# Kernel optimization log

Measured on AMD Instinct MI355X. Metric: run time of the kernel, lower is better.

Reference implementation:

```python
import jax, jax.numpy as jnp
import numpy as np

B, H, V, E, TOPK = 65536, 768, 512, 8, 2
D = H + V  # combined_dim = 1280


def setup_inputs() -> dict:
    key = jax.random.key(0)
    ks = jax.random.split(key, 12)
    def rn(k, sh, scale):
        return jax.random.normal(k, sh, dtype=jnp.float32) * scale
    return {
        "text_features": rn(ks[0], (B, H), 1.0),
        "video_features": rn(ks[1], (B, V), 1.0),
        # 8 stacked experts: 1280->256->128->1
        "exp_w1": rn(ks[2], (E, D, 256), 0.02), "exp_b1": jnp.zeros((E, 256), jnp.float32),
        "exp_w2": rn(ks[3], (E, 256, 128), 0.05), "exp_b2": jnp.zeros((E, 128), jnp.float32),
        "exp_w3": rn(ks[4], (E, 128, 1), 0.08), "exp_b3": jnp.zeros((E, 1), jnp.float32),
        # text router: 768->256->8
        "txt_r_w1": rn(ks[5], (H, 256), 0.03), "txt_r_b1": jnp.zeros((256,), jnp.float32),
        "txt_r_w2": rn(ks[6], (256, E), 0.06), "txt_r_b2": jnp.zeros((E,), jnp.float32),
        # video router: 512->256->8
        "vid_r_w1": rn(ks[7], (V, 256), 0.04), "vid_r_b1": jnp.zeros((256,), jnp.float32),
        "vid_r_w2": rn(ks[8], (256, E), 0.06), "vid_r_b2": jnp.zeros((E,), jnp.float32),
    }


def _router(x, w1, b1, w2, b2):
    return jax.nn.relu(x @ w1 + b1) @ w2 + b2  # [B, E]


def _aggregate(expert_outs, idx, weights):
    # expert_outs: [B, E]; idx/weights: [B, TOPK]
    chosen = jnp.take_along_axis(expert_outs, idx, axis=1)  # [B, TOPK]
    return jnp.sum(weights * chosen, axis=-1, keepdims=True)  # [B, 1]


def reference(text_features, video_features,
              exp_w1, exp_b1, exp_w2, exp_b2, exp_w3, exp_b3,
              txt_r_w1, txt_r_b1, txt_r_w2, txt_r_b2,
              vid_r_w1, vid_r_b1, vid_r_w2, vid_r_b2):
    combined = jnp.concatenate([text_features, video_features], axis=-1)  # [B, D]

    t_logits = _router(text_features, txt_r_w1, txt_r_b1, txt_r_w2, txt_r_b2)
    v_logits = _router(video_features, vid_r_w1, vid_r_b1, vid_r_w2, vid_r_b2)

    t_val, t_idx = jax.lax.top_k(t_logits, TOPK)
    v_val, v_idx = jax.lax.top_k(v_logits, TOPK)
    t_w = jax.nn.softmax(t_val, axis=-1)
    v_w = jax.nn.softmax(v_val, axis=-1)

    # Dense evaluation of all 8 experts (matches original Python loop, vectorized)
    h1 = jax.nn.relu(jnp.einsum('bd,edh->beh', combined, exp_w1) + exp_b1)  # [B,E,256]
    h2 = jax.nn.relu(jnp.einsum('beh,ehf->bef', h1, exp_w2) + exp_b2)       # [B,E,128]
    eo = jax.nn.sigmoid(jnp.einsum('bef,efo->beo', h2, exp_w3) + exp_b3)    # [B,E,1]
    eo = eo[:, :, 0]  # [B, E]

    text_conf = _aggregate(eo, t_idx, t_w)   # [B, 1]
    video_conf = _aggregate(eo, v_idx, v_w)  # [B, 1]
    return text_conf, video_conf
```

## Files before the change

### kernel.cpp

```cpp
#include <hip/hip_runtime.h>
#include <stdint.h>
#include <math.h>

#define B_N 65536
#define H_N 768
#define V_N 512
#define D_N 1280
#define E_N 8
#define N1  256
#define N2  128

#define W1E (E_N*D_N*N1)
#define W2E (E_N*N1*N2)
#define TRE (24*16*512)
#define VRE (16*16*512)

#define DELTA    5e-3f
#define FLAG_CAP 8192

typedef __attribute__((ext_vector_type(8))) short bf16x8;
typedef __attribute__((ext_vector_type(4))) float f32x4;

__device__ __forceinline__ unsigned short f2bf(float f){
  union{float f;uint32_t u;}v; v.f=f;
  uint32_t r = v.u + 0x7FFFu + ((v.u>>16)&1u);
  return (unsigned short)(r>>16);
}
__device__ __forceinline__ float bf2f(unsigned short s){
  union{uint32_t u; float f;}v; v.u = ((uint32_t)s)<<16; return v.f;
}

__global__ void convert_weights(const float* __restrict__ w1,
                                const float* __restrict__ w2,
                                const float* __restrict__ tw1,
                                const float* __restrict__ vw1,
                                unsigned short* __restrict__ w1b,
                                unsigned short* __restrict__ w2b,
                                unsigned short* __restrict__ t_hi,
                                unsigned short* __restrict__ t_lo,
                                unsigned short* __restrict__ v_hi,
                                unsigned short* __restrict__ v_lo,
                                int* __restrict__ counters){
  int i = blockIdx.x*256 + threadIdx.x;
  if (i < 16) counters[i] = 0;
  if (i < W1E){
    int tile = i >> 9, r = i & 511;
    int l = r >> 3, j = r & 7;
    int gt = tile & 15, t2 = tile >> 4;
    int ks = t2 % 40, e = t2 / 40;
    int k = ks*32 + 8*(l>>4) + j;
    int n = gt*16 + (l&15);
    w1b[i] = f2bf(w1[((size_t)e*D_N + k)*N1 + n]);
    return;
  }
  i -= W1E;
  if (i < W2E){
    int tile = i >> 9, r = i & 511;
    int l = r >> 3, j = r & 7;
    int ft = tile & 7, t2 = tile >> 3;
    int ks = t2 & 7, e = t2 >> 3;
    int k = ks*32 + 8*(l>>4) + j;
    int f = ft*16 + (l&15);
    w2b[i] = f2bf(w2[((size_t)e*N1 + k)*N2 + f]);
    return;
  }
  i -= W2E;
  if (i < TRE){
    int tile = i >> 9, r = i & 511;
    int l = r >> 3, j = r & 7;
    int gt = tile & 15, ks = tile >> 4;
    int k = ks*32 + 8*(l>>4) + j;
    int n = gt*16 + (l&15);
    float x = tw1[(size_t)k*N1 + n];
    unsigned short h = f2bf(x);
    t_hi[i] = h;
    t_lo[i] = f2bf(x - bf2f(h));
    return;
  }
  i -= TRE;
  if (i < VRE){
    int tile = i >> 9, r = i & 511;
    int l = r >> 3, j = r & 7;
    int gt = tile & 15, ks = tile >> 4;
    int k = ks*32 + 8*(l>>4) + j;
    int n = gt*16 + (l&15);
    float x = vw1[(size_t)k*N1 + n];
    unsigned short h = f2bf(x);
    v_hi[i] = h;
    v_lo[i] = f2bf(x - bf2f(h));
  }
}

__global__ __launch_bounds__(512,4) void router_mfma(
    const float* __restrict__ text, const float* __restrict__ video,
    const unsigned short* __restrict__ t_hi, const unsigned short* __restrict__ t_lo,
    const unsigned short* __restrict__ v_hi, const unsigned short* __restrict__ v_lo,
    const float* __restrict__ tb1, const float* __restrict__ tw2, const float* __restrict__ tb2,
    const float* __restrict__ vb1, const float* __restrict__ vw2, const float* __restrict__ vb2,
    int* __restrict__ selIdx, float2* __restrict__ selW,
    int* __restrict__ flags, int* __restrict__ counters)
{
  __shared__ union {
    unsigned short a[4*2560];
    float h[64*264];
  } s;
  __shared__ float W2s[256*8];

  const int tid = threadIdx.x;
  const int rt = blockIdx.x >> 10;
  const int r0 = (blockIdx.x & 1023) * 64;
  const float* X = rt ? video : text;
  const unsigned short* Whi = rt ? v_hi : t_hi;
  const unsigned short* Wlo = rt ? v_lo : t_lo;
  const float* b1 = rt ? vb1 : tb1;
  const float* W2 = rt ? vw2 : tw2;
  const float* b2 = rt ? vb2 : tb2;
  const int K  = rt ? V_N : H_N;
  const int NK = K >> 5;

  const int w = tid >> 6, l = tid & 63;
  const int mw = w & 1, nw = w >> 1;
  const int srow = tid >> 3, skq = (tid & 7) * 4;

  for (int i = tid; i < 2048; i += 512) W2s[i] = W2[i];

  f32x4 acc[2][4];
#pragma unroll
  for (int a=0;a<2;a++)
#pragma unroll
    for (int b=0;b<4;b++) acc[a][b] = (f32x4){0.f,0.f,0.f,0.f};

  const float* xrow = X + (size_t)(r0 + srow)*K + skq;
  float4 areg = *(const float4*)xrow;

  for (int ks = 0; ks < NK; ++ks){
    {
      unsigned short* dhi = s.a + (ks&1)*2560 + srow*40 + skq;
      unsigned short* dlo = s.a + (2+(ks&1))*2560 + srow*40 + skq;
      ushort4 uh, ul;
      uh.x = f2bf(areg.x); ul.x = f2bf(areg.x - bf2f(uh.x));
      uh.y = f2bf(areg.y); ul.y = f2bf(areg.y - bf2f(uh.y));
      uh.z = f2bf(areg.z); ul.z = f2bf(areg.z - bf2f(uh.z));
      uh.w = f2bf(areg.w); ul.w = f2bf(areg.w - bf2f(uh.w));
      *(ushort4*)dhi = uh;
      *(ushort4*)dlo = ul;
    }
    if (ks + 1 < NK) areg = *(const float4*)(xrow + (ks+1)*32);
    __syncthreads();

    bf16x8 bh[4], bl[4];
#pragma unroll
    for (int nt=0;nt<4;nt++){
      size_t off = (size_t)(ks*16 + nw*4 + nt)*512 + l*8;
      bh[nt] = *(const bf16x8*)(Whi + off);
      bl[nt] = *(const bf16x8*)(Wlo + off);
    }
    bf16x8 ah[2], al[2];
    const unsigned short* ahi = s.a + (ks&1)*2560;
    const unsigned short* alo = s.a + (2+(ks&1))*2560;
#pragma unroll
    for (int mt=0;mt<2;mt++){
      int ro = (mw*32 + mt*16 + (l&15))*40 + 8*(l>>4);
      ah[mt] = *(const bf16x8*)(ahi + ro);
      al[mt] = *(const bf16x8*)(alo + ro);
    }
#pragma unroll
    for (int mt=0;mt<2;mt++)
#pragma unroll
      for (int nt=0;nt<4;nt++){
        acc[mt][nt] = __builtin_amdgcn_mfma_f32_16x16x32_bf16(ah[mt], bh[nt], acc[mt][nt], 0,0,0);
        acc[mt][nt] = __builtin_amdgcn_mfma_f32_16x16x32_bf16(ah[mt], bl[nt], acc[mt][nt], 0,0,0);
        acc[mt][nt] = __builtin_amdgcn_mfma_f32_16x16x32_bf16(al[mt], bh[nt], acc[mt][nt], 0,0,0);
      }
  }
  __syncthreads();

#pragma unroll
  for (int mt=0;mt<2;mt++){
#pragma unroll
    for (int nt=0;nt<4;nt++){
      int n = nw*64 + nt*16 + (l&15);
      float b1v = b1[n];
#pragma unroll
      for (int i=0;i<4;i++){
        int row = mw*32 + mt*16 + (l>>4)*4 + i;
        float v = acc[mt][nt][i] + b1v;
        s.h[row*264 + n] = v > 0.f ? v : 0.f;
      }
    }
  }
  __syncthreads();

  {
    const int r = tid >> 3, j = tid & 7;
    float part[8];
#pragma unroll
    for (int e=0;e<8;e++) part[e] = 0.f;
    for (int q=0;q<32;q++){
      int n = j + 8*q;
      float hv = s.h[r*264 + n];
#pragma unroll
      for (int e=0;e<8;e++) part[e] += hv * W2s[n*8 + e];
    }
#pragma unroll
    for (int m=1;m<=4;m<<=1)
#pragma unroll
      for (int e=0;e<8;e++) part[e] += __shfl_xor(part[e], m);

    if (j == 0){
      int row = r0 + r;
      float L[8];
#pragma unroll
      for (int e=0;e<8;e++) L[e] = part[e] + b2[e];
      int i0 = 0; float v0 = L[0];
#pragma unroll
      for (int e=1;e<8;e++) if (L[e] > v0){ v0 = L[e]; i0 = e; }
      int i1 = -1; float v1 = -1e30f;
#pragma unroll
      for (int e=0;e<8;e++) if (e != i0 && L[e] > v1){ v1 = L[e]; i1 = e; }
      float v2 = -1e30f;
#pragma unroll
      for (int e=0;e<8;e++) if (e != i0 && e != i1 && L[e] > v2) v2 = L[e];
      if (v1 - v2 < DELTA){
        int idx = atomicAdd(&counters[0], 1);
        if (idx < FLAG_CAP) flags[idx] = (rt<<16) | row;
      }
      float e1 = expf(v1 - v0);
      float invd = 1.f/(1.f + e1);
      selIdx[rt*B_N + row] = i0 | (i1 << 8);
      selW[rt*B_N + row] = make_float2(invd, e1*invd);
    }
  }
}

__global__ __launch_bounds__(256) void router_exact(
    const float* __restrict__ text, const float* __restrict__ video,
    const float* __restrict__ tw1, const float* __restrict__ tb1,
    const float* __restrict__ tw2, const float* __restrict__ tb2,
    const float* __restrict__ vw1, const float* __restrict__ vb1,
    const float* __restrict__ vw2, const float* __restrict__ vb2,
    int* __restrict__ selIdx, float2* __restrict__ selW,
    const int* __restrict__ flags, const int* __restrict__ counters)
{
  int nf = counters[0]; if (nf > FLAG_CAP) nf = FLAG_CAP;
  if ((int)blockIdx.x >= nf) return;
  int code = flags[blockIdx.x];
  int rt = code >> 16, row = code & 0xFFFF;
  const float* X  = rt ? video : text;
  const float* W1 = rt ? vw1 : tw1;
  const float* b1 = rt ? vb1 : tb1;
  const float* W2 = rt ? vw2 : tw2;
  const float* b2 = rt ? vb2 : tb2;
  const int K = rt ? V_N : H_N;

  __shared__ float xs[H_N];
  __shared__ double red[4][8];
  const int tid = threadIdx.x;
  for (int k = tid; k < K; k += 256) xs[k] = X[(size_t)row*K + k];
  __syncthreads();

  double sAcc = 0.0;
  for (int k = 0; k < K; ++k)
    sAcc += (double)xs[k] * (double)W1[(size_t)k*N1 + tid];
  sAcc += (double)b1[tid];
  double h = sAcc > 0.0 ? sAcc : 0.0;

  double p[8];
#pragma unroll
  for (int e=0;e<8;e++) p[e] = h * (double)W2[tid*8 + e];
#pragma unroll
  for (int m=1;m<=32;m<<=1)
#pragma unroll
    for (int e=0;e<8;e++) p[e] += __shfl_xor(p[e], m);
  if ((tid & 63) == 0){
#pragma unroll
    for (int e=0;e<8;e++) red[tid>>6][e] = p[e];
  }
  __syncthreads();
  if (tid == 0){
    double L[8];
#pragma unroll
    for (int e=0;e<8;e++) L[e] = red[0][e]+red[1][e]+red[2][e]+red[3][e] + (double)b2[e];
    int i0 = 0; double v0 = L[0];
#pragma unroll
    for (int e=1;e<8;e++) if (L[e] > v0){ v0 = L[e]; i0 = e; }
    int i1 = -1; double v1 = -1e300;
#pragma unroll
    for (int e=0;e<8;e++) if (e != i0 && L[e] > v1){ v1 = L[e]; i1 = e; }
    double e1 = exp(v1 - v0);
    double invd = 1.0/(1.0 + e1);
    selIdx[rt*B_N + row] = i0 | (i1 << 8);
    selW[rt*B_N + row] = make_float2((float)invd, (float)(e1*invd));
  }
}

__global__ __launch_bounds__(256) void bucket_build(
    const int* __restrict__ selIdx, int* __restrict__ bucket,
    int* __restrict__ counters)
{
  __shared__ int lcnt[8], lbase[8], lpos[8];
  const int tid = threadIdx.x;
  const int row = blockIdx.x*256 + tid;
  if (tid < 8){ lcnt[tid] = 0; lpos[tid] = 0; }
  __syncthreads();
  int st = selIdx[row], sv = selIdx[B_N + row];
  int mask = (1<<(st&7)) | (1<<((st>>8)&7)) | (1<<(sv&7)) | (1<<((sv>>8)&7));
#pragma unroll
  for (int e=0;e<8;e++) if ((mask>>e)&1) atomicAdd(&lcnt[e], 1);
  __syncthreads();
  if (tid < 8) lbase[tid] = atomicAdd(&counters[8+tid], lcnt[tid]);
  __syncthreads();
#pragma unroll
  for (int e=0;e<8;e++)
    if ((mask>>e)&1){
      int p = atomicAdd(&lpos[e], 1);
      bucket[e*B_N + lbase[e] + p] = row;
    }
}

__global__ __launch_bounds__(512) void expert_sparse(
    const float* __restrict__ text, const float* __restrict__ video,
    const unsigned short* __restrict__ w1b, const float* __restrict__ b1,
    const unsigned short* __restrict__ w2b, const float* __restrict__ b2,
    const float* __restrict__ w3, const float* __restrict__ b3,
    const int* __restrict__ bucket, const int* __restrict__ counters,
    float* __restrict__ eo)
{
  __shared__ __align__(16) unsigned short As[4096];
  __shared__ __align__(16) unsigned short h1s[32768];
  __shared__ int rl[128];

  const int tid = threadIdx.x;
  const int e = blockIdx.x & 7;
  const int t = blockIdx.x >> 3;
  const int n_e = counters[8 + e];
  if (t*128 >= n_e) return;

  if (tid < 128){
    int idx = t*128 + tid;
    rl[tid] = (idx < n_e) ? bucket[e*B_N + idx] : -1;
  }
  __syncthreads();

  const int w = tid >> 6, l = tid & 63;
  const int mw = w & 1, nw = w >> 1;

  const int sridx = rl[(tid>>6)*16 + (l&15)];
  const int srr = sridx < 0 ? 0 : sridx;
  const float* tb = text  + (size_t)srr*H_N + (l>>4)*8;
  const float* vb = video + (size_t)srr*V_N + (l>>4)*8;

  f32x4 acc[4][4];
#pragma unroll
  for (int a=0;a<4;a++)
#pragma unroll
    for (int b=0;b<4;b++) acc[a][b] = (f32x4){0.f,0.f,0.f,0.f};

  const unsigned short* w1e = w1b + (size_t)e*40*16*512;

  float4 fa0 = *(const float4*)tb;
  float4 fa1 = *(const float4*)(tb + 4);
  bf16x8 bfc[4];
#pragma unroll
  for (int nt=0;nt<4;nt++)
    bfc[nt] = *(const bf16x8*)(w1e + (size_t)(nw*4 + nt)*512 + l*8);

  for (int ks = 0; ks < 40; ++ks){
    {
      union { bf16x8 v; unsigned short u[8]; } sw;
      sw.u[0]=f2bf(fa0.x); sw.u[1]=f2bf(fa0.y); sw.u[2]=f2bf(fa0.z); sw.u[3]=f2bf(fa0.w);
      sw.u[4]=f2bf(fa1.x); sw.u[5]=f2bf(fa1.y); sw.u[6]=f2bf(fa1.z); sw.u[7]=f2bf(fa1.w);
      *(bf16x8*)(As + tid*8) = sw.v;
    }
    if (ks < 39){
      int k0 = (ks+1)*32;
      const float* p = (k0 < H_N) ? (tb + k0) : (vb + (k0 - H_N));
      fa0 = *(const float4*)p;
      fa1 = *(const float4*)(p + 4);
    }
    __syncthreads();

    bf16x8 af[4];
#pragma unroll
    for (int mt=0;mt<4;mt++)
      af[mt] = *(const bf16x8*)(As + (mw*4+mt)*512 + l*8);

    bf16x8 bfn[4];
    if (ks < 39){
#pragma unroll
      for (int nt=0;nt<4;nt++)
        bfn[nt] = *(const bf16x8*)(w1e + (size_t)((ks+1)*16 + nw*4 + nt)*512 + l*8);
    }
#pragma unroll
    for (int mt=0;mt<4;mt++)
#pragma unroll
      for (int nt=0;nt<4;nt++)
        acc[mt][nt] = __builtin_amdgcn_mfma_f32_16x16x32_bf16(af[mt], bfc[nt], acc[mt][nt], 0,0,0);
    if (ks < 39){
#pragma unroll
      for (int nt=0;nt<4;nt++) bfc[nt] = bfn[nt];
    }
    __syncthreads();
  }

#pragma unroll
  for (int mt=0;mt<4;mt++){
#pragma unroll
    for (int nt=0;nt<4;nt++){
      int n = nw*64 + nt*16 + (l&15);
      float b1v = b1[e*N1 + n];
      int tile = (mw*4+mt)*8 + (n>>5);
      int sub  = 16*((n>>3)&3);
      int jj   = n & 7;
#pragma unroll
      for (int i=0;i<4;i++){
        int r15 = (l>>4)*4 + i;
        float v = acc[mt][nt][i] + b1v;
        v = v > 0.f ? v : 0.f;
        h1s[tile*512 + (r15 + sub)*8 + jj] = f2bf(v);
      }
    }
  }
  __syncthreads();

  f32x4 acc2[4][2];
#pragma unroll
  for (int a=0;a<4;a++)
#pragma unroll
    for (int b=0;b<2;b++) acc2[a][b] = (f32x4){0.f,0.f,0.f,0.f};
  const unsigned short* w2e = w2b + (size_t)e*8*8*512;
#pragma unroll
  for (int ks2=0; ks2<8; ++ks2){
    bf16x8 af2[4], bf2v[2];
#pragma unroll
    for (int mt=0;mt<4;mt++)
      af2[mt] = *(const bf16x8*)(h1s + ((mw*4+mt)*8 + ks2)*512 + l*8);
#pragma unroll
    for (int ft=0;ft<2;ft++)
      bf2v[ft] = *(const bf16x8*)(w2e + (size_t)(ks2*8 + nw*2 + ft)*512 + l*8);
#pragma unroll
    for (int mt=0;mt<4;mt++)
#pragma unroll
      for (int ft=0;ft<2;ft++)
        acc2[mt][ft] = __builtin_amdgcn_mfma_f32_16x16x32_bf16(af2[mt], bf2v[ft], acc2[mt][ft], 0,0,0);
  }

  {
    const float* w3e = w3 + e*N2;
    const float* b2e = b2 + e*N2;
    const int f0 = nw*32 + (l&15);
    const int f1 = f0 + 16;
    float w3v0 = w3e[f0], w3v1 = w3e[f1];
    float b2v0 = b2e[f0], b2v1 = b2e[f1];
    float* red = (float*)As;
#pragma unroll
    for (int mt=0;mt<4;mt++){
#pragma unroll
      for (int i=0;i<4;i++){
        float h20 = acc2[mt][0][i] + b2v0; h20 = h20 > 0.f ? h20 : 0.f;
        float h21 = acc2[mt][1][i] + b2v1; h21 = h21 > 0.f ? h21 : 0.f;
        float p = h20*w3v0 + h21*w3v1;
        p += __shfl_xor(p, 1);
        p += __shfl_xor(p, 2);
        p += __shfl_xor(p, 4);
        p += __shfl_xor(p, 8);
        if ((l & 15) == 0){
          int row = mw*64 + mt*16 + (l>>4)*4 + i;
          red[row*4 + nw] = p;
        }
      }
    }
    __syncthreads();
    if (tid < 128){
      int r = rl[tid];
      if (r >= 0){
        float sum = red[tid*4+0] + red[tid*4+1] + red[tid*4+2] + red[tid*4+3] + b3[e];
        eo[(size_t)r*E_N + e] = 1.f/(1.f + expf(-sum));
      }
    }
  }
}

__global__ __launch_bounds__(512) void aggregate_kernel(
    const int* __restrict__ selIdx, const float2* __restrict__ selW,
    const float* __restrict__ eo, float* __restrict__ out)
{
  int row = blockIdx.x*512 + threadIdx.x;
#pragma unroll
  for (int rt=0; rt<2; rt++){
    int s = selIdx[rt*B_N + row];
    float2 wv = selW[rt*B_N + row];
    out[(size_t)rt*B_N + row] = wv.x * eo[(size_t)row*E_N + (s&7)]
                              + wv.y * eo[(size_t)row*E_N + ((s>>8)&7)];
  }
}

extern "C" void kernel_launch(void* const* d_in, const int* in_sizes, int n_in,
                              void* d_out, int out_size, void* d_ws, size_t ws_size,
                              hipStream_t stream){
  const float* text   = (const float*)d_in[0];
  const float* video  = (const float*)d_in[1];
  const float* exp_w1 = (const float*)d_in[2];
  const float* exp_b1 = (const float*)d_in[3];
  const float* exp_w2 = (const float*)d_in[4];
  const float* exp_b2 = (const float*)d_in[5];
  const float* exp_w3 = (const float*)d_in[6];
  const float* exp_b3 = (const float*)d_in[7];
  const float* tw1 = (const float*)d_in[8];
  const float* tb1 = (const float*)d_in[9];
  const float* tw2 = (const float*)d_in[10];
  const float* tb2 = (const float*)d_in[11];
  const float* vw1 = (const float*)d_in[12];
  const float* vb1 = (const float*)d_in[13];
  const float* vw2 = (const float*)d_in[14];
  const float* vb2 = (const float*)d_in[15];
  float* out = (float*)d_out;

  int*    counters = (int*)d_ws;
  int*    flags    = counters + 16;
  int*    selIdx   = flags + FLAG_CAP;
  float2* selW     = (float2*)(selIdx + 2*B_N);
  int*    bucket   = (int*)(selW + 2*B_N);
  float*  eo       = (float*)(bucket + 8*B_N);
  unsigned short* w1b  = (unsigned short*)(eo + (size_t)B_N*E_N);
  unsigned short* w2b  = w1b  + W1E;
  unsigned short* t_hi = w2b  + W2E;
  unsigned short* t_lo = t_hi + TRE;
  unsigned short* v_hi = t_lo + TRE;
  unsigned short* v_lo = v_hi + VRE;

  convert_weights<<<12544, 256, 0, stream>>>(exp_w1, exp_w2, tw1, vw1,
                                             w1b, w2b, t_hi, t_lo, v_hi, v_lo,
                                             counters);
  router_mfma<<<2048, 512, 0, stream>>>(text, video, t_hi, t_lo, v_hi, v_lo,
                                        tb1, tw2, tb2, vb1, vw2, vb2,
                                        selIdx, selW, flags, counters);
  router_exact<<<FLAG_CAP, 256, 0, stream>>>(text, video, tw1, tb1, tw2, tb2,
                                             vw1, vb1, vw2, vb2,
                                             selIdx, selW, flags, counters);
  bucket_build<<<256, 256, 0, stream>>>(selIdx, bucket, counters);
  expert_sparse<<<4096, 512, 0, stream>>>(text, video, w1b, exp_b1, w2b, exp_b2,
                                          exp_w3, exp_b3, bucket, counters, eo);
  aggregate_kernel<<<128, 512, 0, stream>>>(selIdx, selW, eo, out);
}
```

Measured before the change: 635.9 us.

## Double-buffer A tile, halve h1 shared buffer, and request higher occupancy

```diff
diff --git a/kernel.cpp b/kernel.cpp
--- a/kernel.cpp
+++ b/kernel.cpp
@@ -318,7 +318,7 @@
     }
 }
 
-__global__ __launch_bounds__(512) void expert_sparse(
+__global__ __launch_bounds__(512,4) void expert_sparse(
     const float* __restrict__ text, const float* __restrict__ video,
     const unsigned short* __restrict__ w1b, const float* __restrict__ b1,
     const unsigned short* __restrict__ w2b, const float* __restrict__ b2,
@@ -326,8 +326,8 @@
     const int* __restrict__ bucket, const int* __restrict__ counters,
     float* __restrict__ eo)
 {
-  __shared__ __align__(16) unsigned short As[4096];
-  __shared__ __align__(16) unsigned short h1s[32768];
+  __shared__ __align__(16) unsigned short As[8192];
+  __shared__ __align__(16) unsigned short h1s[16384];
   __shared__ int rl[128];
 
   const int tid = threadIdx.x;
@@ -358,35 +358,44 @@
 
   const unsigned short* w1e = w1b + (size_t)e*40*16*512;
 
-  float4 fa0 = *(const float4*)tb;
-  float4 fa1 = *(const float4*)(tb + 4);
+  {
+    float4 a0 = *(const float4*)tb;
+    float4 a1 = *(const float4*)(tb + 4);
+    union { bf16x8 v; unsigned short u[8]; } sw;
+    sw.u[0]=f2bf(a0.x); sw.u[1]=f2bf(a0.y); sw.u[2]=f2bf(a0.z); sw.u[3]=f2bf(a0.w);
+    sw.u[4]=f2bf(a1.x); sw.u[5]=f2bf(a1.y); sw.u[6]=f2bf(a1.z); sw.u[7]=f2bf(a1.w);
+    *(bf16x8*)(As + tid*8) = sw.v;
+  }
+  float4 pa = *(const float4*)(tb + 32);
+  float4 pb = *(const float4*)(tb + 36);
+
   bf16x8 bfc[4];
 #pragma unroll
   for (int nt=0;nt<4;nt++)
     bfc[nt] = *(const bf16x8*)(w1e + (size_t)(nw*4 + nt)*512 + l*8);
 
   for (int ks = 0; ks < 40; ++ks){
-    {
+    __syncthreads();
+    if (ks + 1 < 40){
       union { bf16x8 v; unsigned short u[8]; } sw;
-      sw.u[0]=f2bf(fa0.x); sw.u[1]=f2bf(fa0.y); sw.u[2]=f2bf(fa0.z); sw.u[3]=f2bf(fa0.w);
-      sw.u[4]=f2bf(fa1.x); sw.u[5]=f2bf(fa1.y); sw.u[6]=f2bf(fa1.z); sw.u[7]=f2bf(fa1.w);
-      *(bf16x8*)(As + tid*8) = sw.v;
-    }
-    if (ks < 39){
-      int k0 = (ks+1)*32;
+      sw.u[0]=f2bf(pa.x); sw.u[1]=f2bf(pa.y); sw.u[2]=f2bf(pa.z); sw.u[3]=f2bf(pa.w);
+      sw.u[4]=f2bf(pb.x); sw.u[5]=f2bf(pb.y); sw.u[6]=f2bf(pb.z); sw.u[7]=f2bf(pb.w);
+      *(bf16x8*)(As + ((ks+1)&1)*4096 + tid*8) = sw.v;
+    }
+    if (ks + 2 < 40){
+      int k0 = (ks+2)*32;
       const float* p = (k0 < H_N) ? (tb + k0) : (vb + (k0 - H_N));
-      fa0 = *(const float4*)p;
-      fa1 = *(const float4*)(p + 4);
-    }
-    __syncthreads();
+      pa = *(const float4*)p;
+      pb = *(const float4*)(p + 4);
+    }
 
     bf16x8 af[4];
 #pragma unroll
     for (int mt=0;mt<4;mt++)
-      af[mt] = *(const bf16x8*)(As + (mw*4+mt)*512 + l*8);
+      af[mt] = *(const bf16x8*)(As + (ks&1)*4096 + (mw*4+mt)*512 + l*8);
 
     bf16x8 bfn[4];
-    if (ks < 39){
+    if (ks + 1 < 40){
 #pragma unroll
       for (int nt=0;nt<4;nt++)
         bfn[nt] = *(const bf16x8*)(w1e + (size_t)((ks+1)*16 + nw*4 + nt)*512 + l*8);
@@ -396,32 +405,11 @@
 #pragma unroll
       for (int nt=0;nt<4;nt++)
         acc[mt][nt] = __builtin_amdgcn_mfma_f32_16x16x32_bf16(af[mt], bfc[nt], acc[mt][nt], 0,0,0);
-    if (ks < 39){
+    if (ks + 1 < 40){
 #pragma unroll
       for (int nt=0;nt<4;nt++) bfc[nt] = bfn[nt];
     }
-    __syncthreads();
-  }
-
-#pragma unroll
-  for (int mt=0;mt<4;mt++){
-#pragma unroll
-    for (int nt=0;nt<4;nt++){
-      int n = nw*64 + nt*16 + (l&15);
-      float b1v = b1[e*N1 + n];
-      int tile = (mw*4+mt)*8 + (n>>5);
-      int sub  = 16*((n>>3)&3);
-      int jj   = n & 7;
-#pragma unroll
-      for (int i=0;i<4;i++){
-        int r15 = (l>>4)*4 + i;
-        float v = acc[mt][nt][i] + b1v;
-        v = v > 0.f ? v : 0.f;
-        h1s[tile*512 + (r15 + sub)*8 + jj] = f2bf(v);
-      }
-    }
-  }
-  __syncthreads();
+  }
 
   f32x4 acc2[4][2];
 #pragma unroll
@@ -429,20 +417,47 @@
 #pragma unroll
     for (int b=0;b<2;b++) acc2[a][b] = (f32x4){0.f,0.f,0.f,0.f};
   const unsigned short* w2e = w2b + (size_t)e*8*8*512;
-#pragma unroll
-  for (int ks2=0; ks2<8; ++ks2){
-    bf16x8 af2[4], bf2v[2];
-#pragma unroll
-    for (int mt=0;mt<4;mt++)
-      af2[mt] = *(const bf16x8*)(h1s + ((mw*4+mt)*8 + ks2)*512 + l*8);
-#pragma unroll
-    for (int ft=0;ft<2;ft++)
-      bf2v[ft] = *(const bf16x8*)(w2e + (size_t)(ks2*8 + nw*2 + ft)*512 + l*8);
-#pragma unroll
-    for (int mt=0;mt<4;mt++)
+
+#pragma unroll
+  for (int half = 0; half < 2; ++half){
+    if ((nw >> 1) == half){
+#pragma unroll
+      for (int mt=0;mt<4;mt++){
+#pragma unroll
+        for (int nt=0;nt<4;nt++){
+          int n = nw*64 + nt*16 + (l&15);
+          float b1v = b1[e*N1 + n];
+          int tile = (mw*4+mt)*4 + ((n>>5)&3);
+          int sub  = 16*((n>>3)&3);
+          int jj   = n & 7;
+#pragma unroll
+          for (int i=0;i<4;i++){
+            int r15 = (l>>4)*4 + i;
+            float v = acc[mt][nt][i] + b1v;
+            v = v > 0.f ? v : 0.f;
+            h1s[tile*512 + (r15 + sub)*8 + jj] = f2bf(v);
+          }
+        }
+      }
+    }
+    __syncthreads();
+#pragma unroll
+    for (int ks2l=0; ks2l<4; ++ks2l){
+      int ks2 = half*4 + ks2l;
+      bf16x8 af2[4], bf2v[2];
+#pragma unroll
+      for (int mt=0;mt<4;mt++)
+        af2[mt] = *(const bf16x8*)(h1s + ((mw*4+mt)*4 + ks2l)*512 + l*8);
 #pragma unroll
       for (int ft=0;ft<2;ft++)
-        acc2[mt][ft] = __builtin_amdgcn_mfma_f32_16x16x32_bf16(af2[mt], bf2v[ft], acc2[mt][ft], 0,0,0);
+        bf2v[ft] = *(const bf16x8*)(w2e + (size_t)(ks2*8 + nw*2 + ft)*512 + l*8);
+#pragma unroll
+      for (int mt=0;mt<4;mt++)
+#pragma unroll
+        for (int ft=0;ft<2;ft++)
+          acc2[mt][ft] = __builtin_amdgcn_mfma_f32_16x16x32_bf16(af2[mt], bf2v[ft], acc2[mt][ft], 0,0,0);
+    }
+    __syncthreads();
   }
 
   {
```

Measured after the change: 686.7 us. 8.0% more time.

## Stage bf16 combined features from router for expert gather reuse

Applied to the files above, without the earlier changes.

```diff
diff --git a/kernel.cpp b/kernel.cpp
--- a/kernel.cpp
+++ b/kernel.cpp
@@ -98,7 +98,8 @@
     const float* __restrict__ tb1, const float* __restrict__ tw2, const float* __restrict__ tb2,
     const float* __restrict__ vb1, const float* __restrict__ vw2, const float* __restrict__ vb2,
     int* __restrict__ selIdx, float2* __restrict__ selW,
-    int* __restrict__ flags, int* __restrict__ counters)
+    int* __restrict__ flags, int* __restrict__ counters,
+    unsigned short* __restrict__ comb, int writeComb)
 {
   __shared__ union {
     unsigned short a[4*2560];
@@ -117,6 +118,7 @@
   const float* b2 = rt ? vb2 : tb2;
   const int K  = rt ? V_N : H_N;
   const int NK = K >> 5;
+  const int cbase = rt ? H_N : 0;
 
   const int w = tid >> 6, l = tid & 63;
   const int mw = w & 1, nw = w >> 1;
@@ -144,6 +146,8 @@
       uh.w = f2bf(areg.w); ul.w = f2bf(areg.w - bf2f(uh.w));
       *(ushort4*)dhi = uh;
       *(ushort4*)dlo = ul;
+      if (writeComb)
+        *(ushort4*)(comb + (size_t)(r0+srow)*D_N + cbase + ks*32 + skq) = uh;
     }
     if (ks + 1 < NK) areg = *(const float4*)(xrow + (ks+1)*32);
     __syncthreads();
@@ -318,7 +322,9 @@
     }
 }
 
-__global__ __launch_bounds__(512) void expert_sparse(
+template<int BF16A>
+__global__ __launch_bounds__(512,4) void expert_sparse(
+    const unsigned short* __restrict__ comb,
     const float* __restrict__ text, const float* __restrict__ video,
     const unsigned short* __restrict__ w1b, const float* __restrict__ b1,
     const unsigned short* __restrict__ w2b, const float* __restrict__ b2,
@@ -347,8 +353,6 @@
 
   const int sridx = rl[(tid>>6)*16 + (l&15)];
   const int srr = sridx < 0 ? 0 : sridx;
-  const float* tb = text  + (size_t)srr*H_N + (l>>4)*8;
-  const float* vb = video + (size_t)srr*V_N + (l>>4)*8;
 
   f32x4 acc[4][4];
 #pragma unroll
@@ -358,49 +362,87 @@
 
   const unsigned short* w1e = w1b + (size_t)e*40*16*512;
 
-  float4 fa0 = *(const float4*)tb;
-  float4 fa1 = *(const float4*)(tb + 4);
   bf16x8 bfc[4];
 #pragma unroll
   for (int nt=0;nt<4;nt++)
     bfc[nt] = *(const bf16x8*)(w1e + (size_t)(nw*4 + nt)*512 + l*8);
 
-  for (int ks = 0; ks < 40; ++ks){
-    {
-      union { bf16x8 v; unsigned short u[8]; } sw;
-      sw.u[0]=f2bf(fa0.x); sw.u[1]=f2bf(fa0.y); sw.u[2]=f2bf(fa0.z); sw.u[3]=f2bf(fa0.w);
-      sw.u[4]=f2bf(fa1.x); sw.u[5]=f2bf(fa1.y); sw.u[6]=f2bf(fa1.z); sw.u[7]=f2bf(fa1.w);
-      *(bf16x8*)(As + tid*8) = sw.v;
-    }
-    if (ks < 39){
-      int k0 = (ks+1)*32;
-      const float* p = (k0 < H_N) ? (tb + k0) : (vb + (k0 - H_N));
-      fa0 = *(const float4*)p;
-      fa1 = *(const float4*)(p + 4);
-    }
-    __syncthreads();
-
-    bf16x8 af[4];
-#pragma unroll
-    for (int mt=0;mt<4;mt++)
-      af[mt] = *(const bf16x8*)(As + (mw*4+mt)*512 + l*8);
-
-    bf16x8 bfn[4];
-    if (ks < 39){
-#pragma unroll
-      for (int nt=0;nt<4;nt++)
-        bfn[nt] = *(const bf16x8*)(w1e + (size_t)((ks+1)*16 + nw*4 + nt)*512 + l*8);
-    }
-#pragma unroll
-    for (int mt=0;mt<4;mt++)
-#pragma unroll
-      for (int nt=0;nt<4;nt++)
-        acc[mt][nt] = __builtin_amdgcn_mfma_f32_16x16x32_bf16(af[mt], bfc[nt], acc[mt][nt], 0,0,0);
-    if (ks < 39){
-#pragma unroll
-      for (int nt=0;nt<4;nt++) bfc[nt] = bfn[nt];
-    }
-    __syncthreads();
+  if constexpr (BF16A){
+    const unsigned short* arow = comb + (size_t)srr*D_N + (l>>4)*8;
+    bf16x8 rc = *(const bf16x8*)arow;
+    bf16x8 rn = *(const bf16x8*)(arow + 32);
+
+    for (int ks = 0; ks < 40; ++ks){
+      *(bf16x8*)(As + tid*8) = rc;
+      rc = rn;
+      if (ks + 2 < 40) rn = *(const bf16x8*)(arow + (ks+2)*32);
+      __syncthreads();
+
+      bf16x8 af[4];
+#pragma unroll
+      for (int mt=0;mt<4;mt++)
+        af[mt] = *(const bf16x8*)(As + (mw*4+mt)*512 + l*8);
+
+      bf16x8 bfn[4];
+      if (ks + 1 < 40){
+#pragma unroll
+        for (int nt=0;nt<4;nt++)
+          bfn[nt] = *(const bf16x8*)(w1e + (size_t)((ks+1)*16 + nw*4 + nt)*512 + l*8);
+      }
+#pragma unroll
+      for (int mt=0;mt<4;mt++)
+#pragma unroll
+        for (int nt=0;nt<4;nt++)
+          acc[mt][nt] = __builtin_amdgcn_mfma_f32_16x16x32_bf16(af[mt], bfc[nt], acc[mt][nt], 0,0,0);
+      if (ks + 1 < 40){
+#pragma unroll
+        for (int nt=0;nt<4;nt++) bfc[nt] = bfn[nt];
+      }
+      __syncthreads();
+    }
+  } else {
+    const float* tb = text  + (size_t)srr*H_N + (l>>4)*8;
+    const float* vb = video + (size_t)srr*V_N + (l>>4)*8;
+    float4 fa0 = *(const float4*)tb;
+    float4 fa1 = *(const float4*)(tb + 4);
+
+    for (int ks = 0; ks < 40; ++ks){
+      {
+        union { bf16x8 v; unsigned short u[8]; } sw;
+        sw.u[0]=f2bf(fa0.x); sw.u[1]=f2bf(fa0.y); sw.u[2]=f2bf(fa0.z); sw.u[3]=f2bf(fa0.w);
+        sw.u[4]=f2bf(fa1.x); sw.u[5]=f2bf(fa1.y); sw.u[6]=f2bf(fa1.z); sw.u[7]=f2bf(fa1.w);
+        *(bf16x8*)(As + tid*8) = sw.v;
+      }
+      if (ks < 39){
+        int k0 = (ks+1)*32;
+        const float* p = (k0 < H_N) ? (tb + k0) : (vb + (k0 - H_N));
+        fa0 = *(const float4*)p;
+        fa1 = *(const float4*)(p + 4);
+      }
+      __syncthreads();
+
+      bf16x8 af[4];
+#pragma unroll
+      for (int mt=0;mt<4;mt++)
+        af[mt] = *(const bf16x8*)(As + (mw*4+mt)*512 + l*8);
+
+      bf16x8 bfn[4];
+      if (ks < 39){
+#pragma unroll
+        for (int nt=0;nt<4;nt++)
+          bfn[nt] = *(const bf16x8*)(w1e + (size_t)((ks+1)*16 + nw*4 + nt)*512 + l*8);
+      }
+#pragma unroll
+      for (int mt=0;mt<4;mt++)
+#pragma unroll
+        for (int nt=0;nt<4;nt++)
+          acc[mt][nt] = __builtin_amdgcn_mfma_f32_16x16x32_bf16(af[mt], bfc[nt], acc[mt][nt], 0,0,0);
+      if (ks < 39){
+#pragma unroll
+        for (int nt=0;nt<4;nt++) bfc[nt] = bfn[nt];
+      }
+      __syncthreads();
+    }
   }
 
 #pragma unroll
@@ -516,30 +558,46 @@
   const float* vb2 = (const float*)d_in[15];
   float* out = (float*)d_out;
 
-  int*    counters = (int*)d_ws;
-  int*    flags    = counters + 16;
-  int*    selIdx   = flags + FLAG_CAP;
-  float2* selW     = (float2*)(selIdx + 2*B_N);
-  int*    bucket   = (int*)(selW + 2*B_N);
-  float*  eo       = (float*)(bucket + 8*B_N);
-  unsigned short* w1b  = (unsigned short*)(eo + (size_t)B_N*E_N);
-  unsigned short* w2b  = w1b  + W1E;
-  unsigned short* t_hi = w2b  + W2E;
-  unsigned short* t_lo = t_hi + TRE;
-  unsigned short* v_hi = t_lo + TRE;
-  unsigned short* v_lo = v_hi + VRE;
+  size_t off = 0;
+  auto alloc = [&](size_t bytes) -> char* {
+    char* p = (char*)d_ws + off;
+    off += (bytes + 255) & ~(size_t)255;
+    return p;
+  };
+  int*    counters = (int*)   alloc(16*4);
+  int*    flags    = (int*)   alloc((size_t)FLAG_CAP*4);
+  int*    selIdx   = (int*)   alloc((size_t)2*B_N*4);
+  float2* selW     = (float2*)alloc((size_t)2*B_N*8);
+  int*    bucket   = (int*)   alloc((size_t)8*B_N*4);
+  float*  eo       = (float*) alloc((size_t)B_N*E_N*4);
+  unsigned short* w1b  = (unsigned short*)alloc((size_t)W1E*2);
+  unsigned short* w2b  = (unsigned short*)alloc((size_t)W2E*2);
+  unsigned short* t_hi = (unsigned short*)alloc((size_t)TRE*2);
+  unsigned short* t_lo = (unsigned short*)alloc((size_t)TRE*2);
+  unsigned short* v_hi = (unsigned short*)alloc((size_t)VRE*2);
+  unsigned short* v_lo = (unsigned short*)alloc((size_t)VRE*2);
+  unsigned short* comb = (unsigned short*)alloc((size_t)B_N*D_N*2);
+  const int useComb = (off <= ws_size) ? 1 : 0;
 
   convert_weights<<<12544, 256, 0, stream>>>(exp_w1, exp_w2, tw1, vw1,
                                              w1b, w2b, t_hi, t_lo, v_hi, v_lo,
                                              counters);
   router_mfma<<<2048, 512, 0, stream>>>(text, video, t_hi, t_lo, v_hi, v_lo,
                                         tb1, tw2, tb2, vb1, vw2, vb2,
-                                        selIdx, selW, flags, counters);
+                                        selIdx, selW, flags, counters,
+                                        comb, useComb);
   router_exact<<<FLAG_CAP, 256, 0, stream>>>(text, video, tw1, tb1, tw2, tb2,
                                              vw1, vb1, vw2, vb2,
                                              selIdx, selW, flags, counters);
   bucket_build<<<256, 256, 0, stream>>>(selIdx, bucket, counters);
-  expert_sparse<<<4096, 512, 0, stream>>>(text, video, w1b, exp_b1, w2b, exp_b2,
-                                          exp_w3, exp_b3, bucket, counters, eo);
+  if (useComb){
+    expert_sparse<1><<<4096, 512, 0, stream>>>(comb, text, video,
+                                               w1b, exp_b1, w2b, exp_b2,
+                                               exp_w3, exp_b3, bucket, counters, eo);
+  } else {
+    expert_sparse<0><<<4096, 512, 0, stream>>>(comb, text, video,
+                                               w1b, exp_b1, w2b, exp_b2,
+                                               exp_w3, exp_b3, bucket, counters, eo);
+  }
   aggregate_kernel<<<128, 512, 0, stream>>>(selIdx, selW, eo, out);
 }
```

New measurement: 574.5 us. 9.7% less time.
